# Kernel optimization log

Hardware: AMD Instinct MI355X
Metric: run time of the kernel (lower is better)

## Reference

```python
import jax, jax.numpy as jnp
import numpy as np

N_POINTS = 1_000_000
FDIM = 32
GRID = 128  # gx = gy = gz = ceil(20 / 0.15625) = 128
LO, HI = -10.0, 10.0
INIT_STD = 0.05


def setup_inputs() -> dict:
    key = jax.random.key(0)
    k1, k2 = jax.random.split(key)
    # query points inside the bound
    x = jax.random.uniform(k1, (N_POINTS, 3), jnp.float32, LO, HI)
    # dense voxel feature grid, layout [C, D, H, W] (squeezed batch dim)
    feature = jax.random.normal(k2, (FDIM, GRID, GRID, GRID), jnp.float32) * INIT_STD
    return {"x": x, "feature": feature}


def reference(x, feature):
    # normalize_coordinates: map bound -> [-1, 1] per axis (x, y, z order)
    coords = 2.0 * (x - LO) / (HI - LO) - 1.0  # [N, 3]

    C, D, H, W = feature.shape
    # grid_sample, align_corners=False: pixel = ((c + 1) * size - 1) / 2
    fx = ((coords[:, 0] + 1.0) * W - 1.0) * 0.5
    fy = ((coords[:, 1] + 1.0) * H - 1.0) * 0.5
    fz = ((coords[:, 2] + 1.0) * D - 1.0) * 0.5

    x0f, y0f, z0f = jnp.floor(fx), jnp.floor(fy), jnp.floor(fz)
    wx, wy, wz = fx - x0f, fy - y0f, fz - z0f  # trilinear fractions
    x0 = x0f.astype(jnp.int32)
    y0 = y0f.astype(jnp.int32)
    z0 = z0f.astype(jnp.int32)

    feat_flat = feature.reshape(C, -1)  # [C, D*H*W]
    out = jnp.zeros((C, x.shape[0]), dtype=feature.dtype)
    for dz in (0, 1):
        for dy in (0, 1):
            for dx in (0, 1):
                xi, yi, zi = x0 + dx, y0 + dy, z0 + dz
                w = ((wx if dx else 1.0 - wx)
                     * (wy if dy else 1.0 - wy)
                     * (wz if dz else 1.0 - wz))
                # padding_mode='zeros': out-of-range corners contribute 0
                valid = ((xi >= 0) & (xi < W) & (yi >= 0) & (yi < H)
                         & (zi >= 0) & (zi < D))
                idx = ((jnp.clip(zi, 0, D - 1) * H + jnp.clip(yi, 0, H - 1)) * W
                       + jnp.clip(xi, 0, W - 1))
                vals = feat_flat[:, idx]  # gather -> [C, N]
                out = out + vals * (w * valid).astype(feature.dtype)[None, :]
    # transpose(0, 1) -> [N, fdim]
    return out.T
```

## Files before the change

kernel.cpp:

```cpp
#include <hip/hip_runtime.h>
#include <hip/hip_fp16.h>


constexpr int   GD      = 128;
constexpr long long SPATIAL = (long long)GD * GD * GD;
constexpr int   FD      = 32;
constexpr float PLO     = -10.0f;
constexpr float PHI     = 10.0f;
constexpr int   NBUCKET = 129;

typedef float nfloat4 __attribute__((ext_vector_type(4)));

__device__ __forceinline__ int z_bucket(float pz) {
    const float cz = 2.0f * (pz - PLO) / (PHI - PLO) - 1.0f;
    const float fz = ((cz + 1.0f) * GD - 1.0f) * 0.5f;
    int zb = (int)floorf(fz) + 1;
    return min(max(zb, 0), NBUCKET - 1);
}

__global__ __launch_bounds__(256) void transpose_feat_h(
    const float* __restrict__ f, __half* __restrict__ o) {
    __shared__ float lds[64][FD + 1];
    const int t  = threadIdx.x;
    const long long s0 = (long long)blockIdx.x * 64;
    const int sl = t & 63;
    const int cq = t >> 6;
#pragma unroll
    for (int it = 0; it < 8; ++it) {
        const int c = it * 4 + cq;
        lds[sl][c] =
            __builtin_nontemporal_load(f + (size_t)c * SPATIAL + s0 + sl);
    }
    __syncthreads();
    const int c0 = (t & 15) * 2;
    const int sw = t >> 4;
#pragma unroll
    for (int it = 0; it < 4; ++it) {
        const int s = sw + it * 16;
        __half2 h;
        h.x = __float2half(lds[s][c0]);
        h.y = __float2half(lds[s][c0 + 1]);
        *reinterpret_cast<__half2*>(o + (size_t)(s0 + s) * FD + c0) = h;
    }
}

__global__ __launch_bounds__(256) void hist_blocks(
    const float* __restrict__ x, int* __restrict__ blockHist,
    int npts, int nblocks) {
    __shared__ int h[NBUCKET];
    const int t = threadIdx.x;
    if (t < NBUCKET) h[t] = 0;
    __syncthreads();
    const int n = blockIdx.x * 256 + t;
    if (n < npts) atomicAdd(&h[z_bucket(x[3 * n + 2])], 1);
    __syncthreads();
    if (t < NBUCKET)
        blockHist[(size_t)t * nblocks + blockIdx.x] = h[t];
}

__global__ __launch_bounds__(256) void scan_bins(
    int* __restrict__ blockHist, int* __restrict__ binSum, int nblocks) {
    __shared__ int tmp[256];
    const int bin = blockIdx.x;
    int* row = blockHist + (size_t)bin * nblocks;
    const int t = threadIdx.x;
    int carry = 0;
    for (int base = 0; base < nblocks; base += 256) {
        const int i = base + t;
        const int v = (i < nblocks) ? row[i] : 0;
        tmp[t] = v;
        __syncthreads();
        int run = v;
        for (int off = 1; off < 256; off <<= 1) {
            const int add = (t >= off) ? tmp[t - off] : 0;
            __syncthreads();
            run += add;
            tmp[t] = run;
            __syncthreads();
        }
        if (i < nblocks) row[i] = carry + (run - v);
        carry += tmp[255];
        __syncthreads();
    }
    if (t == 0) binSum[bin] = carry;
}

__global__ void scan_bin_totals(const int* __restrict__ binSum,
                                int* __restrict__ binBase) {
    if (threadIdx.x == 0 && blockIdx.x == 0) {
        int run = 0;
        for (int b = 0; b < NBUCKET; ++b) {
            binBase[b] = run;
            run += binSum[b];
        }
    }
}

__global__ __launch_bounds__(256) void scatter_det(
    const float* __restrict__ x, const int* __restrict__ blockHist,
    const int* __restrict__ binBase, nfloat4* __restrict__ binned,
    int npts, int nblocks) {
    __shared__ int h[NBUCKET];
    const int t = threadIdx.x;
    if (t < NBUCKET) h[t] = 0;
    __syncthreads();
    const int n = blockIdx.x * 256 + t;
    if (n >= npts) return;
    const float px = x[3 * n + 0];
    const float py = x[3 * n + 1];
    const float pz = x[3 * n + 2];
    const int bin = z_bucket(pz);
    const int rank = atomicAdd(&h[bin], 1);
    const int dest =
        binBase[bin] + blockHist[(size_t)bin * nblocks + blockIdx.x] + rank;
    nfloat4 rec = {px, py, pz, __int_as_float(n)};
    binned[dest] = rec;
}

__global__ __launch_bounds__(256) void trilerp_b(
    const nfloat4* __restrict__ binned, const __half* __restrict__ ft,
    float* __restrict__ out, int npts) {
    const int tid = blockIdx.x * 256 + threadIdx.x;
    const int i = tid >> 2;
    if (i >= npts) return;
    const int j = tid & 3;

    const nfloat4 rec = binned[i];
    const float px = rec.x, py = rec.y, pz = rec.z;
    const int n = __float_as_int(rec.w);

    const float cx = 2.0f * (px - PLO) / (PHI - PLO) - 1.0f;
    const float cy = 2.0f * (py - PLO) / (PHI - PLO) - 1.0f;
    const float cz = 2.0f * (pz - PLO) / (PHI - PLO) - 1.0f;
    const float fx = ((cx + 1.0f) * GD - 1.0f) * 0.5f;
    const float fy = ((cy + 1.0f) * GD - 1.0f) * 0.5f;
    const float fz = ((cz + 1.0f) * GD - 1.0f) * 0.5f;

    const float x0f = floorf(fx), y0f = floorf(fy), z0f = floorf(fz);
    const float wx = fx - x0f, wy = fy - y0f, wz = fz - z0f;
    const int x0 = (int)x0f, y0 = (int)y0f, z0 = (int)z0f;

    float acc[8] = {0.f, 0.f, 0.f, 0.f, 0.f, 0.f, 0.f, 0.f};
#pragma unroll
    for (int dz = 0; dz < 2; ++dz) {
#pragma unroll
        for (int dy = 0; dy < 2; ++dy) {
#pragma unroll
            for (int dx = 0; dx < 2; ++dx) {
                const int xi = x0 + dx, yi = y0 + dy, zi = z0 + dz;
                const bool valid = ((unsigned)xi < (unsigned)GD) &
                                   ((unsigned)yi < (unsigned)GD) &
                                   ((unsigned)zi < (unsigned)GD);
                float w = (dx ? wx : 1.0f - wx) * (dy ? wy : 1.0f - wy) *
                          (dz ? wz : 1.0f - wz);
                w = valid ? w : 0.0f;
                const int xc = min(max(xi, 0), GD - 1);
                const int yc = min(max(yi, 0), GD - 1);
                const int zc = min(max(zi, 0), GD - 1);
                const size_t idx = (size_t)(zc * GD + yc) * GD + xc;
                const nfloat4 raw = *reinterpret_cast<const nfloat4*>(
                    ft + idx * FD + j * 8);
                const __half2* h2 = reinterpret_cast<const __half2*>(&raw);
#pragma unroll
                for (int k = 0; k < 4; ++k) {
                    const float2 fv = __half22float2(h2[k]);
                    acc[2 * k + 0] = fmaf(fv.x, w, acc[2 * k + 0]);
                    acc[2 * k + 1] = fmaf(fv.y, w, acc[2 * k + 1]);
                }
            }
        }
    }
    float* op = out + (size_t)n * FD + j * 8;
    nfloat4 o0 = {acc[0], acc[1], acc[2], acc[3]};
    nfloat4 o1 = {acc[4], acc[5], acc[6], acc[7]};
    __builtin_nontemporal_store(o0, reinterpret_cast<nfloat4*>(op));
    __builtin_nontemporal_store(o1, reinterpret_cast<nfloat4*>(op) + 1);
}

__global__ __launch_bounds__(256) void trilerp_h(
    const float* __restrict__ x, const __half* __restrict__ ft,
    float* __restrict__ out, int npts) {
    const int tid = blockIdx.x * 256 + threadIdx.x;
    const int n = tid >> 2;
    if (n >= npts) return;
    const int j = tid & 3;

    const float px = x[3 * n + 0];
    const float py = x[3 * n + 1];
    const float pz = x[3 * n + 2];
    const float cx = 2.0f * (px - PLO) / (PHI - PLO) - 1.0f;
    const float cy = 2.0f * (py - PLO) / (PHI - PLO) - 1.0f;
    const float cz = 2.0f * (pz - PLO) / (PHI - PLO) - 1.0f;
    const float fx = ((cx + 1.0f) * GD - 1.0f) * 0.5f;
    const float fy = ((cy + 1.0f) * GD - 1.0f) * 0.5f;
    const float fz = ((cz + 1.0f) * GD - 1.0f) * 0.5f;
    const float x0f = floorf(fx), y0f = floorf(fy), z0f = floorf(fz);
    const float wx = fx - x0f, wy = fy - y0f, wz = fz - z0f;
    const int x0 = (int)x0f, y0 = (int)y0f, z0 = (int)z0f;

    float acc[8] = {0.f, 0.f, 0.f, 0.f, 0.f, 0.f, 0.f, 0.f};
#pragma unroll
    for (int dz = 0; dz < 2; ++dz)
#pragma unroll
        for (int dy = 0; dy < 2; ++dy)
#pragma unroll
            for (int dx = 0; dx < 2; ++dx) {
                const int xi = x0 + dx, yi = y0 + dy, zi = z0 + dz;
                const bool valid = ((unsigned)xi < (unsigned)GD) &
                                   ((unsigned)yi < (unsigned)GD) &
                                   ((unsigned)zi < (unsigned)GD);
                float w = (dx ? wx : 1.0f - wx) * (dy ? wy : 1.0f - wy) *
                          (dz ? wz : 1.0f - wz);
                w = valid ? w : 0.0f;
                const int xc = min(max(xi, 0), GD - 1);
                const int yc = min(max(yi, 0), GD - 1);
                const int zc = min(max(zi, 0), GD - 1);
                const size_t idx = (size_t)(zc * GD + yc) * GD + xc;
                const nfloat4 raw = *reinterpret_cast<const nfloat4*>(
                    ft + idx * FD + j * 8);
                const __half2* h2 = reinterpret_cast<const __half2*>(&raw);
#pragma unroll
                for (int k = 0; k < 4; ++k) {
                    const float2 fv = __half22float2(h2[k]);
                    acc[2 * k + 0] = fmaf(fv.x, w, acc[2 * k + 0]);
                    acc[2 * k + 1] = fmaf(fv.y, w, acc[2 * k + 1]);
                }
            }
    float* op = out + (size_t)n * FD + j * 8;
    nfloat4 o0 = {acc[0], acc[1], acc[2], acc[3]};
    nfloat4 o1 = {acc[4], acc[5], acc[6], acc[7]};
    __builtin_nontemporal_store(o0, reinterpret_cast<nfloat4*>(op));
    __builtin_nontemporal_store(o1, reinterpret_cast<nfloat4*>(op) + 1);
}

__global__ __launch_bounds__(256) void trilerp_direct(
    const float* __restrict__ x, const float* __restrict__ f,
    float* __restrict__ out, int npts) {
    const int tid = blockIdx.x * 256 + threadIdx.x;
    const int n = tid >> 3;
    if (n >= npts) return;
    const int j = tid & 7;

    const float px = x[3 * n + 0];
    const float py = x[3 * n + 1];
    const float pz = x[3 * n + 2];
    const float cx = 2.0f * (px - PLO) / (PHI - PLO) - 1.0f;
    const float cy = 2.0f * (py - PLO) / (PHI - PLO) - 1.0f;
    const float cz = 2.0f * (pz - PLO) / (PHI - PLO) - 1.0f;
    const float fx = ((cx + 1.0f) * GD - 1.0f) * 0.5f;
    const float fy = ((cy + 1.0f) * GD - 1.0f) * 0.5f;
    const float fz = ((cz + 1.0f) * GD - 1.0f) * 0.5f;
    const float x0f = floorf(fx), y0f = floorf(fy), z0f = floorf(fz);
    const float wx = fx - x0f, wy = fy - y0f, wz = fz - z0f;
    const int x0 = (int)x0f, y0 = (int)y0f, z0 = (int)z0f;

    float acc[4] = {0.f, 0.f, 0.f, 0.f};
#pragma unroll
    for (int dz = 0; dz < 2; ++dz)
#pragma unroll
        for (int dy = 0; dy < 2; ++dy)
#pragma unroll
            for (int dx = 0; dx < 2; ++dx) {
                const int xi = x0 + dx, yi = y0 + dy, zi = z0 + dz;
                const bool valid = ((unsigned)xi < (unsigned)GD) &
                                   ((unsigned)yi < (unsigned)GD) &
                                   ((unsigned)zi < (unsigned)GD);
                float w = (dx ? wx : 1.0f - wx) * (dy ? wy : 1.0f - wy) *
                          (dz ? wz : 1.0f - wz);
                w = valid ? w : 0.0f;
                const int xc = min(max(xi, 0), GD - 1);
                const int yc = min(max(yi, 0), GD - 1);
                const int zc = min(max(zi, 0), GD - 1);
                const size_t idx = (size_t)(zc * GD + yc) * GD + xc;
#pragma unroll
                for (int k = 0; k < 4; ++k)
                    acc[k] = fmaf(f[(size_t)(j * 4 + k) * SPATIAL + idx], w, acc[k]);
            }
#pragma unroll
    for (int k = 0; k < 4; ++k) out[(size_t)n * FD + j * 4 + k] = acc[k];
}

extern "C" void kernel_launch(void* const* d_in, const int* in_sizes, int n_in,
                              void* d_out, int out_size, void* d_ws, size_t ws_size,
                              hipStream_t stream) {
    const float* x    = (const float*)d_in[0];
    const float* feat = (const float*)d_in[1];
    float*       out  = (float*)d_out;
    const int npts = in_sizes[0] / 3;

    const int nb      = (npts + 255) / 256;
    const int gblocks = (npts * 4 + 255) / 256;

    const size_t FTH_BYTES    = (size_t)SPATIAL * FD * sizeof(__half);
    const size_t BINNED_OFF   = FTH_BYTES;
    const size_t BINNED_BYTES = (size_t)npts * 16;
    const size_t BH_OFF  = BINNED_OFF + ((BINNED_BYTES + 255) & ~(size_t)255);
    const size_t BH_BYTES = (size_t)NBUCKET * nb * sizeof(int);
    const size_t META_OFF = BH_OFF + ((BH_BYTES + 255) & ~(size_t)255);
    const size_t META_BYTES = 2 * NBUCKET * sizeof(int);
    const size_t need_binned = META_OFF + META_BYTES;

    if (ws_size >= need_binned) {
        __half*  fth    = (__half*)d_ws;
        nfloat4* binned = (nfloat4*)((char*)d_ws + BINNED_OFF);
        int*     bhist  = (int*)((char*)d_ws + BH_OFF);
        int*     binSum = (int*)((char*)d_ws + META_OFF);
        int*     binBase = binSum + NBUCKET;

        transpose_feat_h<<<(int)(SPATIAL / 64), 256, 0, stream>>>(feat, fth);
        hist_blocks<<<nb, 256, 0, stream>>>(x, bhist, npts, nb);
        scan_bins<<<NBUCKET, 256, 0, stream>>>(bhist, binSum, nb);
        scan_bin_totals<<<1, 64, 0, stream>>>(binSum, binBase);
        scatter_det<<<nb, 256, 0, stream>>>(x, bhist, binBase, binned, npts, nb);
        trilerp_b<<<gblocks, 256, 0, stream>>>(binned, fth, out, npts);
    } else if (ws_size >= FTH_BYTES) {
        __half* fth = (__half*)d_ws;
        transpose_feat_h<<<(int)(SPATIAL / 64), 256, 0, stream>>>(feat, fth);
        trilerp_h<<<gblocks, 256, 0, stream>>>(x, fth, out, npts);
    } else {
        const int dblocks = (npts * 8 + 255) / 256;
        trilerp_direct<<<dblocks, 256, 0, stream>>>(x, feat, out, npts);
    }
}
```

Baseline: 508.1 us.

## Bin points into 3D bricks and trilerp from an LDS-staged feature brick

Replaces the 1D z-slab binning with 3D binning into 17^3 bricks of 8^3 cells. Each trilerp block now stages a 9^3 halo brick of the fp16 transposed feature grid in LDS and interpolates its bin's points from shared memory instead of gathering from global memory. This aims to cut repeated global gathers and improve locality. In exchange there are more, heavier histogram and scan steps (4913 bins times 512 blocks), and the brick load cost is fixed per bin, so very unevenly filled bins could unbalance the work.

```diff
diff --git a/kernel.cpp b/kernel.cpp
--- a/kernel.cpp
+++ b/kernel.cpp
@@ -7,15 +7,34 @@
 constexpr int   FD      = 32;
 constexpr float PLO     = -10.0f;
 constexpr float PHI     = 10.0f;
-constexpr int   NBUCKET = 129;
+
+constexpr int   NBX     = 17;
+constexpr int   NBINS   = NBX * NBX * NBX;
+constexpr int   HBLK    = 512;
+constexpr int   VS      = 9;
+constexpr int   VN      = VS * VS * VS;
+constexpr int   VSTRIDE = 80;
 
 typedef float nfloat4 __attribute__((ext_vector_type(4)));
 
-__device__ __forceinline__ int z_bucket(float pz) {
+__device__ __forceinline__ void cell_of(float px, float py, float pz,
+                                        int& x0, int& y0, int& z0) {
+    const float cx = 2.0f * (px - PLO) / (PHI - PLO) - 1.0f;
+    const float cy = 2.0f * (py - PLO) / (PHI - PLO) - 1.0f;
     const float cz = 2.0f * (pz - PLO) / (PHI - PLO) - 1.0f;
+    const float fx = ((cx + 1.0f) * GD - 1.0f) * 0.5f;
+    const float fy = ((cy + 1.0f) * GD - 1.0f) * 0.5f;
     const float fz = ((cz + 1.0f) * GD - 1.0f) * 0.5f;
-    int zb = (int)floorf(fz) + 1;
-    return min(max(zb, 0), NBUCKET - 1);
+    x0 = (int)floorf(fx);
+    y0 = (int)floorf(fy);
+    z0 = (int)floorf(fz);
+}
+
+__device__ __forceinline__ int bin_of(int x0, int y0, int z0) {
+    const int bx = min(max((x0 + 1) >> 3, 0), NBX - 1);
+    const int by = min(max((y0 + 1) >> 3, 0), NBX - 1);
+    const int bz = min(max((z0 + 1) >> 3, 0), NBX - 1);
+    return (bz * NBX + by) * NBX + bx;
 }
 
 __global__ __launch_bounds__(256) void transpose_feat_h(
@@ -44,30 +63,32 @@
     }
 }
 
-__global__ __launch_bounds__(256) void hist_blocks(
-    const float* __restrict__ x, int* __restrict__ blockHist,
-    int npts, int nblocks) {
-    __shared__ int h[NBUCKET];
-    const int t = threadIdx.x;
-    if (t < NBUCKET) h[t] = 0;
-    __syncthreads();
-    const int n = blockIdx.x * 256 + t;
-    if (n < npts) atomicAdd(&h[z_bucket(x[3 * n + 2])], 1);
-    __syncthreads();
-    if (t < NBUCKET)
-        blockHist[(size_t)t * nblocks + blockIdx.x] = h[t];
-}
-
-__global__ __launch_bounds__(256) void scan_bins(
-    int* __restrict__ blockHist, int* __restrict__ binSum, int nblocks) {
+__global__ __launch_bounds__(256) void hist3d(
+    const float* __restrict__ x, int* __restrict__ blockHist, int npts) {
+    __shared__ int h[NBINS];
+    const int t = threadIdx.x;
+    for (int i = t; i < NBINS; i += 256) h[i] = 0;
+    __syncthreads();
+    const int stride = gridDim.x * 256;
+    for (int n = blockIdx.x * 256 + t; n < npts; n += stride) {
+        int x0, y0, z0;
+        cell_of(x[3 * n + 0], x[3 * n + 1], x[3 * n + 2], x0, y0, z0);
+        atomicAdd(&h[bin_of(x0, y0, z0)], 1);
+    }
+    __syncthreads();
+    int* row = blockHist + (size_t)blockIdx.x * NBINS;
+    for (int i = t; i < NBINS; i += 256) row[i] = h[i];
+}
+
+__global__ __launch_bounds__(256) void scan_rows(
+    int* __restrict__ blockHist, int* __restrict__ binSum, int nblk) {
     __shared__ int tmp[256];
     const int bin = blockIdx.x;
-    int* row = blockHist + (size_t)bin * nblocks;
     const int t = threadIdx.x;
     int carry = 0;
-    for (int base = 0; base < nblocks; base += 256) {
-        const int i = base + t;
-        const int v = (i < nblocks) ? row[i] : 0;
+    for (int base = 0; base < nblk; base += 256) {
+        const int blk = base + t;
+        const int v = (blk < nblk) ? blockHist[(size_t)blk * NBINS + bin] : 0;
         tmp[t] = v;
         __syncthreads();
         int run = v;
@@ -78,73 +99,174 @@
             tmp[t] = run;
             __syncthreads();
         }
-        if (i < nblocks) row[i] = carry + (run - v);
+        if (blk < nblk) blockHist[(size_t)blk * NBINS + bin] = carry + (run - v);
         carry += tmp[255];
         __syncthreads();
     }
     if (t == 0) binSum[bin] = carry;
 }
 
-__global__ void scan_bin_totals(const int* __restrict__ binSum,
-                                int* __restrict__ binBase) {
-    if (threadIdx.x == 0 && blockIdx.x == 0) {
-        int run = 0;
-        for (int b = 0; b < NBUCKET; ++b) {
-            binBase[b] = run;
-            run += binSum[b];
+__global__ __launch_bounds__(256) void scan_totals(
+    const int* __restrict__ binSum, int* __restrict__ binBase) {
+    __shared__ int tmp[256];
+    const int t = threadIdx.x;
+    int carry = 0;
+    for (int base = 0; base < NBINS; base += 256) {
+        const int i = base + t;
+        const int v = (i < NBINS) ? binSum[i] : 0;
+        tmp[t] = v;
+        __syncthreads();
+        int run = v;
+        for (int off = 1; off < 256; off <<= 1) {
+            const int add = (t >= off) ? tmp[t - off] : 0;
+            __syncthreads();
+            run += add;
+            tmp[t] = run;
+            __syncthreads();
         }
-    }
-}
-
-__global__ __launch_bounds__(256) void scatter_det(
+        if (i < NBINS) binBase[i] = carry + (run - v);
+        carry += tmp[255];
+        __syncthreads();
+    }
+    if (t == 0) binBase[NBINS] = carry;
+}
+
+__global__ __launch_bounds__(256) void scatter3d(
     const float* __restrict__ x, const int* __restrict__ blockHist,
-    const int* __restrict__ binBase, nfloat4* __restrict__ binned,
-    int npts, int nblocks) {
-    __shared__ int h[NBUCKET];
-    const int t = threadIdx.x;
-    if (t < NBUCKET) h[t] = 0;
-    __syncthreads();
-    const int n = blockIdx.x * 256 + t;
+    const int* __restrict__ binBase, nfloat4* __restrict__ binned, int npts) {
+    __shared__ int h[NBINS];
+    const int t = threadIdx.x;
+    for (int i = t; i < NBINS; i += 256) h[i] = 0;
+    __syncthreads();
+    const int* row = blockHist + (size_t)blockIdx.x * NBINS;
+    const int stride = gridDim.x * 256;
+    for (int n = blockIdx.x * 256 + t; n < npts; n += stride) {
+        const float px = x[3 * n + 0];
+        const float py = x[3 * n + 1];
+        const float pz = x[3 * n + 2];
+        int x0, y0, z0;
+        cell_of(px, py, pz, x0, y0, z0);
+        const int bin = bin_of(x0, y0, z0);
+        const int rank = atomicAdd(&h[bin], 1);
+        const int dest = binBase[bin] + row[bin] + rank;
+        nfloat4 rec = {px, py, pz, __int_as_float(n)};
+        binned[dest] = rec;
+    }
+}
+
+__global__ __launch_bounds__(256) void trilerp_lds(
+    const nfloat4* __restrict__ binned, const __half* __restrict__ ft,
+    const int* __restrict__ binBase, float* __restrict__ out) {
+    __shared__ __align__(16) unsigned char smem[VN * VSTRIDE];
+    const int bin = blockIdx.x;
+    const int bx = bin % NBX;
+    const int bq = bin / NBX;
+    const int by = bq % NBX;
+    const int bz = bq / NBX;
+    const int vbx = bx * 8 - 1, vby = by * 8 - 1, vbz = bz * 8 - 1;
+    const int t = threadIdx.x;
+
+    for (int i = t; i < VN * 4; i += 256) {
+        const int v = i >> 2, ch = i & 3;
+        const int lx = v % VS;
+        const int vq = v / VS;
+        const int ly = vq % VS;
+        const int lz = vq / VS;
+        const int gx = min(max(vbx + lx, 0), GD - 1);
+        const int gy = min(max(vby + ly, 0), GD - 1);
+        const int gz = min(max(vbz + lz, 0), GD - 1);
+        const size_t src = ((size_t)(gz * GD + gy) * GD + gx) * FD + ch * 8;
+        *reinterpret_cast<nfloat4*>(&smem[v * VSTRIDE + ch * 16]) =
+            *reinterpret_cast<const nfloat4*>(ft + src);
+    }
+    __syncthreads();
+
+    const int start = binBase[bin];
+    const int end   = binBase[bin + 1];
+    const int j = t & 3;
+
+    for (int p = start + (t >> 2); p < end; p += 64) {
+        const nfloat4 rec = binned[p];
+        const float px = rec.x, py = rec.y, pz = rec.z;
+        const int n = __float_as_int(rec.w);
+
+        const float cx = 2.0f * (px - PLO) / (PHI - PLO) - 1.0f;
+        const float cy = 2.0f * (py - PLO) / (PHI - PLO) - 1.0f;
+        const float cz = 2.0f * (pz - PLO) / (PHI - PLO) - 1.0f;
+        const float fx = ((cx + 1.0f) * GD - 1.0f) * 0.5f;
+        const float fy = ((cy + 1.0f) * GD - 1.0f) * 0.5f;
+        const float fz = ((cz + 1.0f) * GD - 1.0f) * 0.5f;
+
+        const float x0f = floorf(fx), y0f = floorf(fy), z0f = floorf(fz);
+        const float wx = fx - x0f, wy = fy - y0f, wz = fz - z0f;
+        const int x0 = (int)x0f, y0 = (int)y0f, z0 = (int)z0f;
+
+        const int lx0 = min(max(x0 - vbx, 0), VS - 2);
+        const int ly0 = min(max(y0 - vby, 0), VS - 2);
+        const int lz0 = min(max(z0 - vbz, 0), VS - 2);
+
+        float acc[8] = {0.f, 0.f, 0.f, 0.f, 0.f, 0.f, 0.f, 0.f};
+#pragma unroll
+        for (int dz = 0; dz < 2; ++dz) {
+#pragma unroll
+            for (int dy = 0; dy < 2; ++dy) {
+#pragma unroll
+                for (int dx = 0; dx < 2; ++dx) {
+                    const int xi = x0 + dx, yi = y0 + dy, zi = z0 + dz;
+                    const bool valid = ((unsigned)xi < (unsigned)GD) &
+                                       ((unsigned)yi < (unsigned)GD) &
+                                       ((unsigned)zi < (unsigned)GD);
+                    float w = (dx ? wx : 1.0f - wx) * (dy ? wy : 1.0f - wy) *
+                              (dz ? wz : 1.0f - wz);
+                    w = valid ? w : 0.0f;
+                    const int v =
+                        ((lz0 + dz) * VS + (ly0 + dy)) * VS + (lx0 + dx);
+                    const nfloat4 raw = *reinterpret_cast<const nfloat4*>(
+                        &smem[v * VSTRIDE + j * 16]);
+                    const __half2* h2 = reinterpret_cast<const __half2*>(&raw);
+#pragma unroll
+                    for (int k = 0; k < 4; ++k) {
+                        const float2 fv = __half22float2(h2[k]);
+                        acc[2 * k + 0] = fmaf(fv.x, w, acc[2 * k + 0]);
+                        acc[2 * k + 1] = fmaf(fv.y, w, acc[2 * k + 1]);
+                    }
+                }
+            }
+        }
+        float* op = out + (size_t)n * FD + j * 8;
+        nfloat4 o0 = {acc[0], acc[1], acc[2], acc[3]};
+        nfloat4 o1 = {acc[4], acc[5], acc[6], acc[7]};
+        __builtin_nontemporal_store(o0, reinterpret_cast<nfloat4*>(op));
+        __builtin_nontemporal_store(o1, reinterpret_cast<nfloat4*>(op) + 1);
+    }
+}
+
+__global__ __launch_bounds__(256) void trilerp_h(
+    const float* __restrict__ x, const __half* __restrict__ ft,
+    float* __restrict__ out, int npts) {
+    const int tid = blockIdx.x * 256 + threadIdx.x;
+    const int n = tid >> 2;
     if (n >= npts) return;
+    const int j = tid & 3;
+
     const float px = x[3 * n + 0];
     const float py = x[3 * n + 1];
     const float pz = x[3 * n + 2];
-    const int bin = z_bucket(pz);
-    const int rank = atomicAdd(&h[bin], 1);
-    const int dest =
-        binBase[bin] + blockHist[(size_t)bin * nblocks + blockIdx.x] + rank;
-    nfloat4 rec = {px, py, pz, __int_as_float(n)};
-    binned[dest] = rec;
-}
-
-__global__ __launch_bounds__(256) void trilerp_b(
-    const nfloat4* __restrict__ binned, const __half* __restrict__ ft,
-    float* __restrict__ out, int npts) {
-    const int tid = blockIdx.x * 256 + threadIdx.x;
-    const int i = tid >> 2;
-    if (i >= npts) return;
-    const int j = tid & 3;
-
-    const nfloat4 rec = binned[i];
-    const float px = rec.x, py = rec.y, pz = rec.z;
-    const int n = __float_as_int(rec.w);
-
     const float cx = 2.0f * (px - PLO) / (PHI - PLO) - 1.0f;
     const float cy = 2.0f * (py - PLO) / (PHI - PLO) - 1.0f;
     const float cz = 2.0f * (pz - PLO) / (PHI - PLO) - 1.0f;
     const float fx = ((cx + 1.0f) * GD - 1.0f) * 0.5f;
     const float fy = ((cy + 1.0f) * GD - 1.0f) * 0.5f;
     const float fz = ((cz + 1.0f) * GD - 1.0f) * 0.5f;
-
     const float x0f = floorf(fx), y0f = floorf(fy), z0f = floorf(fz);
     const float wx = fx - x0f, wy = fy - y0f, wz = fz - z0f;
     const int x0 = (int)x0f, y0 = (int)y0f, z0 = (int)z0f;
 
     float acc[8] = {0.f, 0.f, 0.f, 0.f, 0.f, 0.f, 0.f, 0.f};
 #pragma unroll
-    for (int dz = 0; dz < 2; ++dz) {
-#pragma unroll
-        for (int dy = 0; dy < 2; ++dy) {
+    for (int dz = 0; dz < 2; ++dz)
+#pragma unroll
+        for (int dy = 0; dy < 2; ++dy)
 #pragma unroll
             for (int dx = 0; dx < 2; ++dx) {
                 const int xi = x0 + dx, yi = y0 + dy, zi = z0 + dz;
@@ -168,8 +290,6 @@
                     acc[2 * k + 1] = fmaf(fv.y, w, acc[2 * k + 1]);
                 }
             }
-        }
-    }
     float* op = out + (size_t)n * FD + j * 8;
     nfloat4 o0 = {acc[0], acc[1], acc[2], acc[3]};
     nfloat4 o1 = {acc[4], acc[5], acc[6], acc[7]};
@@ -177,13 +297,13 @@
     __builtin_nontemporal_store(o1, reinterpret_cast<nfloat4*>(op) + 1);
 }
 
-__global__ __launch_bounds__(256) void trilerp_h(
-    const float* __restrict__ x, const __half* __restrict__ ft,
+__global__ __launch_bounds__(256) void trilerp_direct(
+    const float* __restrict__ x, const float* __restrict__ f,
     float* __restrict__ out, int npts) {
     const int tid = blockIdx.x * 256 + threadIdx.x;
-    const int n = tid >> 2;
+    const int n = tid >> 3;
     if (n >= npts) return;
-    const int j = tid & 3;
+    const int j = tid & 7;
 
     const float px = x[3 * n + 0];
     const float py = x[3 * n + 1];
@@ -198,7 +318,7 @@
     const float wx = fx - x0f, wy = fy - y0f, wz = fz - z0f;
     const int x0 = (int)x0f, y0 = (int)y0f, z0 = (int)z0f;
 
-    float acc[8] = {0.f, 0.f, 0.f, 0.f, 0.f, 0.f, 0.f, 0.f};
+    float acc[4] = {0.f, 0.f, 0.f, 0.f};
 #pragma unroll
     for (int dz = 0; dz < 2; ++dz)
 #pragma unroll
@@ -216,62 +336,6 @@
                 const int yc = min(max(yi, 0), GD - 1);
                 const int zc = min(max(zi, 0), GD - 1);
                 const size_t idx = (size_t)(zc * GD + yc) * GD + xc;
-                const nfloat4 raw = *reinterpret_cast<const nfloat4*>(
-                    ft + idx * FD + j * 8);
-                const __half2* h2 = reinterpret_cast<const __half2*>(&raw);
-#pragma unroll
-                for (int k = 0; k < 4; ++k) {
-                    const float2 fv = __half22float2(h2[k]);
-                    acc[2 * k + 0] = fmaf(fv.x, w, acc[2 * k + 0]);
-                    acc[2 * k + 1] = fmaf(fv.y, w, acc[2 * k + 1]);
-                }
-            }
-    float* op = out + (size_t)n * FD + j * 8;
-    nfloat4 o0 = {acc[0], acc[1], acc[2], acc[3]};
-    nfloat4 o1 = {acc[4], acc[5], acc[6], acc[7]};
-    __builtin_nontemporal_store(o0, reinterpret_cast<nfloat4*>(op));
-    __builtin_nontemporal_store(o1, reinterpret_cast<nfloat4*>(op) + 1);
-}
-
-__global__ __launch_bounds__(256) void trilerp_direct(
-    const float* __restrict__ x, const float* __restrict__ f,
-    float* __restrict__ out, int npts) {
-    const int tid = blockIdx.x * 256 + threadIdx.x;
-    const int n = tid >> 3;
-    if (n >= npts) return;
-    const int j = tid & 7;
-
-    const float px = x[3 * n + 0];
-    const float py = x[3 * n + 1];
-    const float pz = x[3 * n + 2];
-    const float cx = 2.0f * (px - PLO) / (PHI - PLO) - 1.0f;
-    const float cy = 2.0f * (py - PLO) / (PHI - PLO) - 1.0f;
-    const float cz = 2.0f * (pz - PLO) / (PHI - PLO) - 1.0f;
-    const float fx = ((cx + 1.0f) * GD - 1.0f) * 0.5f;
-    const float fy = ((cy + 1.0f) * GD - 1.0f) * 0.5f;
-    const float fz = ((cz + 1.0f) * GD - 1.0f) * 0.5f;
-    const float x0f = floorf(fx), y0f = floorf(fy), z0f = floorf(fz);
-    const float wx = fx - x0f, wy = fy - y0f, wz = fz - z0f;
-    const int x0 = (int)x0f, y0 = (int)y0f, z0 = (int)z0f;
-
-    float acc[4] = {0.f, 0.f, 0.f, 0.f};
-#pragma unroll
-    for (int dz = 0; dz < 2; ++dz)
-#pragma unroll
-        for (int dy = 0; dy < 2; ++dy)
-#pragma unroll
-            for (int dx = 0; dx < 2; ++dx) {
-                const int xi = x0 + dx, yi = y0 + dy, zi = z0 + dz;
-                const bool valid = ((unsigned)xi < (unsigned)GD) &
-                                   ((unsigned)yi < (unsigned)GD) &
-                                   ((unsigned)zi < (unsigned)GD);
-                float w = (dx ? wx : 1.0f - wx) * (dy ? wy : 1.0f - wy) *
-                          (dz ? wz : 1.0f - wz);
-                w = valid ? w : 0.0f;
-                const int xc = min(max(xi, 0), GD - 1);
-                const int yc = min(max(yi, 0), GD - 1);
-                const int zc = min(max(zi, 0), GD - 1);
-                const size_t idx = (size_t)(zc * GD + yc) * GD + xc;
 #pragma unroll
                 for (int k = 0; k < 4; ++k)
                     acc[k] = fmaf(f[(size_t)(j * 4 + k) * SPATIAL + idx], w, acc[k]);
@@ -288,31 +352,32 @@
     float*       out  = (float*)d_out;
     const int npts = in_sizes[0] / 3;
 
-    const int nb      = (npts + 255) / 256;
-    const int gblocks = (npts * 4 + 255) / 256;
-
     const size_t FTH_BYTES    = (size_t)SPATIAL * FD * sizeof(__half);
     const size_t BINNED_OFF   = FTH_BYTES;
     const size_t BINNED_BYTES = (size_t)npts * 16;
-    const size_t BH_OFF  = BINNED_OFF + ((BINNED_BYTES + 255) & ~(size_t)255);
-    const size_t BH_BYTES = (size_t)NBUCKET * nb * sizeof(int);
-    const size_t META_OFF = BH_OFF + ((BH_BYTES + 255) & ~(size_t)255);
-    const size_t META_BYTES = 2 * NBUCKET * sizeof(int);
-    const size_t need_binned = META_OFF + META_BYTES;
+    const size_t BH_OFF   = BINNED_OFF + ((BINNED_BYTES + 255) & ~(size_t)255);
+    const size_t BH_BYTES = (size_t)HBLK * NBINS * sizeof(int);
+    const size_t SUM_OFF  = BH_OFF + ((BH_BYTES + 255) & ~(size_t)255);
+    const size_t SUM_BYTES  = (size_t)NBINS * sizeof(int);
+    const size_t BASE_OFF = SUM_OFF + ((SUM_BYTES + 255) & ~(size_t)255);
+    const size_t BASE_BYTES = (size_t)(NBINS + 1) * sizeof(int);
+    const size_t need_binned = BASE_OFF + BASE_BYTES;
+
+    const int gblocks = (npts * 4 + 255) / 256;
 
     if (ws_size >= need_binned) {
-        __half*  fth    = (__half*)d_ws;
-        nfloat4* binned = (nfloat4*)((char*)d_ws + BINNED_OFF);
-        int*     bhist  = (int*)((char*)d_ws + BH_OFF);
-        int*     binSum = (int*)((char*)d_ws + META_OFF);
-        int*     binBase = binSum + NBUCKET;
+        __half*  fth     = (__half*)d_ws;
+        nfloat4* binned  = (nfloat4*)((char*)d_ws + BINNED_OFF);
+        int*     bhist   = (int*)((char*)d_ws + BH_OFF);
+        int*     binSum  = (int*)((char*)d_ws + SUM_OFF);
+        int*     binBase = (int*)((char*)d_ws + BASE_OFF);
 
         transpose_feat_h<<<(int)(SPATIAL / 64), 256, 0, stream>>>(feat, fth);
-        hist_blocks<<<nb, 256, 0, stream>>>(x, bhist, npts, nb);
-        scan_bins<<<NBUCKET, 256, 0, stream>>>(bhist, binSum, nb);
-        scan_bin_totals<<<1, 64, 0, stream>>>(binSum, binBase);
-        scatter_det<<<nb, 256, 0, stream>>>(x, bhist, binBase, binned, npts, nb);
-        trilerp_b<<<gblocks, 256, 0, stream>>>(binned, fth, out, npts);
+        hist3d<<<HBLK, 256, 0, stream>>>(x, bhist, npts);
+        scan_rows<<<NBINS, 256, 0, stream>>>(bhist, binSum, HBLK);
+        scan_totals<<<1, 256, 0, stream>>>(binSum, binBase);
+        scatter3d<<<HBLK, 256, 0, stream>>>(x, bhist, binBase, binned, npts);
+        trilerp_lds<<<NBINS, 256, 0, stream>>>(binned, fth, binBase, out);
     } else if (ws_size >= FTH_BYTES) {
         __half* fth = (__half*)d_ws;
         transpose_feat_h<<<(int)(SPATIAL / 64), 256, 0, stream>>>(feat, fth);
```

New measurement: 549.4 us. +8.1%, slower.
